# Kernel optimization log

Hardware: AMD Instinct MI355X
Metric: run time of the kernel (lower is better)

## Reference

```python
import jax, jax.numpy as jnp
import numpy as np
from jax import lax

F1, D, F2 = 8, 2, 16
CTX = 64           # context = 1.0 s * 64 Hz
NCH = 64           # EEG channels
POOL1, POOL2 = 2, 5
BN_EPS = 1e-5


def _conv2d(x, w, b, padding, groups=1):
    y = lax.conv_general_dilated(x, w, (1, 1), padding,
                                 dimension_numbers=('NCHW', 'OIHW', 'NCHW'),
                                 feature_group_count=groups)
    return y + b[None, :, None, None]


def _bn(x, g, b, m, v):
    scale = g / jnp.sqrt(v + BN_EPS)
    return (x - m[None, :, None, None]) * scale[None, :, None, None] + b[None, :, None, None]


def _avgpool_w(x, k):
    y = lax.reduce_window(x, jnp.float32(0), lax.add, (1, 1, 1, k), (1, 1, 1, k), 'VALID')
    return y / k


def setup_inputs() -> dict:
    key = jax.random.key(0)
    ks = jax.random.split(key, 24)
    B, C, eegL = 16, NCH, 256
    f32 = jnp.float32
    inp = {
        'eeg': jax.random.normal(ks[0], (B, C, eegL), f32),
        'env': jax.random.normal(ks[1], (B, 2, eegL), f32),
        # conv1: Conv2d(1, F1, (1,3), padding='same')
        'conv1_w': jax.random.normal(ks[2], (F1, 1, 1, 3), f32) * 0.3,
        'conv1_b': jax.random.normal(ks[3], (F1,), f32) * 0.05,
        'bn1_g': jax.random.uniform(ks[4], (F1,), f32, 0.8, 1.2),
        'bn1_b': jax.random.normal(ks[5], (F1,), f32) * 0.05,
        'bn1_m': jax.random.normal(ks[6], (F1,), f32) * 0.1,
        'bn1_v': jax.random.uniform(ks[7], (F1,), f32, 0.5, 1.5),
        # conv2: Conv2d(F1, F1*D, (NCH,1), 'valid', groups=F1)
        'conv2_w': jax.random.normal(ks[8], (F1 * D, 1, NCH, 1), f32) * 0.05,
        'conv2_b': jax.random.normal(ks[9], (F1 * D,), f32) * 0.05,
        'bn2_g': jax.random.uniform(ks[10], (F1 * D,), f32, 0.8, 1.2),
        'bn2_b': jax.random.normal(ks[11], (F1 * D,), f32) * 0.05,
        'bn2_m': jax.random.normal(ks[12], (F1 * D,), f32) * 0.1,
        'bn2_v': jax.random.uniform(ks[13], (F1 * D,), f32, 0.5, 1.5),
        # conv3: depthwise Conv2d(F1*D, F1*D, (1,3), 'same', groups=F1*D)
        'conv3_w': jax.random.normal(ks[14], (F1 * D, 1, 1, 3), f32) * 0.3,
        'conv3_b': jax.random.normal(ks[15], (F1 * D,), f32) * 0.05,
        # conv4: pointwise Conv2d(F1*D, F2, (1,1))
        'conv4_w': jax.random.normal(ks[16], (F2, F1 * D, 1, 1), f32) * 0.2,
        'conv4_b': jax.random.normal(ks[17], (F2,), f32) * 0.05,
        'bn3_g': jax.random.uniform(ks[18], (F2,), f32, 0.8, 1.2),
        'bn3_b': jax.random.normal(ks[19], (F2,), f32) * 0.05,
        'bn3_m': jax.random.normal(ks[20], (F2,), f32) * 0.1,
        'bn3_v': jax.random.uniform(ks[21], (F2,), f32, 0.5, 1.5),
        # linear: F2 * (CTX // (POOL1*POOL2)) -> 1
        'lin_w': jax.random.normal(ks[22], (1, F2 * (CTX // (POOL1 * POOL2))), f32) * 0.1,
        'lin_b': jax.random.normal(ks[23], (1,), f32) * 0.05,
    }
    return inp


def _forward(eeg, conv1_w, conv1_b, bn1_g, bn1_b, bn1_m, bn1_v,
             conv2_w, conv2_b, bn2_g, bn2_b, bn2_m, bn2_v,
             conv3_w, conv3_b, conv4_w, conv4_b,
             bn3_g, bn3_b, bn3_m, bn3_v, lin_w, lin_b):
    B, C, eegL = eeg.shape
    L = eegL - CTX + 1
    # extract all overlapping windows: [B, C, L, CTX] -> [B*L, 1, C, CTX]
    idx = jnp.arange(L)[:, None] + jnp.arange(CTX)[None, :]
    win = eeg[:, :, idx]                      # [B, C, L, CTX]
    x = win.transpose(0, 2, 1, 3).reshape(B * L, 1, C, CTX)
    x = _conv2d(x, conv1_w, conv1_b, ((0, 0), (1, 1)))            # same pad on time
    x = _bn(x, bn1_g, bn1_b, bn1_m, bn1_v)
    x = _conv2d(x, conv2_w, conv2_b, ((0, 0), (0, 0)), groups=F1)  # spatial conv -> H=1
    x = _bn(x, bn2_g, bn2_b, bn2_m, bn2_v)
    x = jax.nn.elu(x)
    x = _avgpool_w(x, POOL1)
    x = _conv2d(x, conv3_w, conv3_b, ((0, 0), (1, 1)), groups=F1 * D)  # depthwise temporal
    x = _conv2d(x, conv4_w, conv4_b, ((0, 0), (0, 0)))                 # pointwise
    x = _bn(x, bn3_g, bn3_b, bn3_m, bn3_v)
    x = jax.nn.elu(x)
    x = _avgpool_w(x, POOL2)
    x = x.reshape(B * L, -1)                  # [B*L, F2*6]
    y = x @ lin_w.T + lin_b                   # [B*L, 1]
    return y.reshape(B, L)


def reference(eeg, env, conv1_w, conv1_b, bn1_g, bn1_b, bn1_m, bn1_v,
              conv2_w, conv2_b, bn2_g, bn2_b, bn2_m, bn2_v,
              conv3_w, conv3_b, conv4_w, conv4_b,
              bn3_g, bn3_b, bn3_m, bn3_v, lin_w, lin_b):
    assert env.shape[1] == 2  # n_streams check (env unused by the math)
    return _forward(eeg, conv1_w, conv1_b, bn1_g, bn1_b, bn1_m, bn1_v,
                    conv2_w, conv2_b, bn2_g, bn2_b, bn2_m, bn2_v,
                    conv3_w, conv3_b, conv4_w, conv4_b,
                    bn3_g, bn3_b, bn3_m, bn3_v, lin_w, lin_b)
```

## Files before the change

### kernel.cpp

```cpp
#include <hip/hip_runtime.h>
#include <math.h>

#define BN_EPS 1e-5f
#define LWIN   193
#define WPB    16
#define NBL    13
#define SLOC   96
#define STR    97

typedef __attribute__((address_space(1))) const unsigned int gl_u32;
typedef __attribute__((address_space(3))) unsigned int lds_u32;

__device__ __forceinline__ float elu(float x) { return x > 0.f ? x : expm1f(x); }

__global__ __launch_bounds__(256) void eegnet_fused(
    const float* __restrict__ eeg,
    const float* __restrict__ c1w, const float* __restrict__ c1b,
    const float* __restrict__ bn1g, const float* __restrict__ bn1b,
    const float* __restrict__ bn1m, const float* __restrict__ bn1v,
    const float* __restrict__ w2,  const float* __restrict__ c2b,
    const float* __restrict__ bn2g, const float* __restrict__ bn2b,
    const float* __restrict__ bn2m, const float* __restrict__ bn2v,
    const float* __restrict__ c3w, const float* __restrict__ c3b,
    const float* __restrict__ c4w, const float* __restrict__ c4b,
    const float* __restrict__ bn3g, const float* __restrict__ bn3b,
    const float* __restrict__ bn3m, const float* __restrict__ bn3v,
    const float* __restrict__ linw, const float* __restrict__ linb,
    float* __restrict__ out)
{
    const int b   = blockIdx.x;
    const int L0  = blockIdx.y * WPB;
    const int g0  = L0 - 3;
    const int tid = threadIdx.x;
    const int lane16 = tid & 15;
    const int grp16  = tid >> 4;

    __shared__ __align__(16) float Eg[64 * SLOC];
    __shared__ float4 w2t4[64 * 4];
    __shared__ float  Ul[16][STR];
    __shared__ float  El[16][STR];
    __shared__ float  P2[16][STR];
    __shared__ float  Ql[16][STR];
    __shared__ float  Ef[16][STR];
    __shared__ float  S5[16][STR];
    __shared__ float  cs[512];
    __shared__ float  q0s[16][17], q1s[16][17];

    const float* ebase = eeg + b * 64 * 256;

    {
        const int wv = tid >> 6, ln = tid & 63;
        #pragma unroll
        for (int j = 0; j < 6; ++j) {
            const int n    = wv * 6 + j;
            const int fidx = n * 256 + ln * 4;
            const int c    = fidx / SLOC;
            const int i    = fidx - c * SLOC;
            const int s    = g0 + i;
            if (s >= 0 && s <= 252) {
                __builtin_amdgcn_global_load_lds((gl_u32*)(ebase + c * 256 + s),
                                                 (lds_u32*)&Eg[n * 256], 16, 0, 0);
            } else {
                const float* row = ebase + c * 256;
                const int e0 = s     < 0 ? 0 : (s     > 255 ? 255 : s);
                const int e1 = s + 1 < 0 ? 0 : (s + 1 > 255 ? 255 : s + 1);
                const int e2 = s + 2 < 0 ? 0 : (s + 2 > 255 ? 255 : s + 2);
                const int e3 = s + 3 < 0 ? 0 : (s + 3 > 255 ? 255 : s + 3);
                *reinterpret_cast<float4*>(&Eg[fidx]) =
                    make_float4(row[e0], row[e1], row[e2], row[e3]);
            }
        }
    }

    {
        const int og = tid >> 6, c = tid & 63, o0 = og * 4;
        w2t4[c * 4 + og] = make_float4(w2[(o0    ) * 64 + c], w2[(o0 + 1) * 64 + c],
                                       w2[(o0 + 2) * 64 + c], w2[(o0 + 3) * 64 + c]);
    }

    if (tid < 64) {
        const int f = tid & 15, q = tid >> 4;
        float s2p = 0.f;
        #pragma unroll
        for (int k = 0; k < 16; ++k) s2p += w2[f * 64 + q * 16 + k];
        s2p += __shfl_xor(s2p, 16);
        s2p += __shfl_xor(s2p, 32);
        if (tid < 16) {
            const int g = f >> 1;
            const float s1 = bn1g[g] / sqrtf(bn1v[g] + BN_EPS);
            const float o1 = bn1b[g] - bn1m[g] * s1;
            const float s2 = bn2g[f] / sqrtf(bn2v[f] + BN_EPS);
            const float o2 = bn2b[f] - bn2m[f] * s2;
            const float ss = s2 * s1;
            cs[      f] = ss * c1w[g * 3 + 0];
            cs[ 16 + f] = ss * c1w[g * 3 + 1];
            cs[ 32 + f] = ss * c1w[g * 3 + 2];
            cs[ 48 + f] = s2 * (fmaf(s1, c1b[g], o1) * s2p + c2b[f]) + o2;
            cs[ 64 + f] = c3w[f * 3 + 0];
            cs[ 80 + f] = c3w[f * 3 + 1];
            cs[ 96 + f] = c3w[f * 3 + 2];
            cs[112 + f] = c3b[f];
        }
    } else if (tid < 128) {
        const int j = tid - 64, f = j & 15, quad = j >> 4;
        const float s3 = bn3g[f] / sqrtf(bn3v[f] + BN_EPS);
        if (quad == 0)
            cs[128 + f] = fmaf(s3, c4b[f], bn3b[f] - bn3m[f] * s3);
        #pragma unroll
        for (int k = 0; k < 4; ++k) {
            const int o = quad * 4 + k;
            cs[144 + o * 16 + f] = s3 * c4w[f * 16 + o];
        }
    } else if (tid < 224) {
        cs[400 + tid - 128] = linw[tid - 128];
    } else if (tid == 224) {
        cs[496] = linb[0];
    }
    __syncthreads();

    {
        const int p  = tid & 63;
        const int og = tid >> 6;
        const bool two = (p < 32);
        float a0 = 0.f, a1 = 0.f, a2 = 0.f, a3 = 0.f;
        float b0 = 0.f, b1 = 0.f, b2 = 0.f, b3 = 0.f;
        #pragma unroll 8
        for (int c = 0; c < 64; ++c) {
            const float4 w = w2t4[c * 4 + og];
            const float  e = Eg[c * SLOC + p];
            a0 = fmaf(w.x, e, a0); a1 = fmaf(w.y, e, a1);
            a2 = fmaf(w.z, e, a2); a3 = fmaf(w.w, e, a3);
            if (two) {
                const float e2 = Eg[c * SLOC + p + 64];
                b0 = fmaf(w.x, e2, b0); b1 = fmaf(w.y, e2, b1);
                b2 = fmaf(w.z, e2, b2); b3 = fmaf(w.w, e2, b3);
            }
        }
        const int o0 = og * 4;
        Ul[o0    ][p] = a0; Ul[o0 + 1][p] = a1;
        Ul[o0 + 2][p] = a2; Ul[o0 + 3][p] = a3;
        if (two) {
            Ul[o0    ][p + 64] = b0; Ul[o0 + 1][p + 64] = b1;
            Ul[o0 + 2][p + 64] = b2; Ul[o0 + 3][p + 64] = b3;
        }
    }
    __syncthreads();

    #pragma unroll
    for (int k = 0; k < 6; ++k) {
        const int i = grp16 + 16 * k, sg = g0 + i, o = lane16;
        const float um = (sg >= 1)   ? Ul[o][i > 0 ? i - 1 : 0] : 0.f;
        const float uc = Ul[o][i];
        const float up = (sg <= 254) ? Ul[o][i < SLOC - 1 ? i + 1 : SLOC - 1] : 0.f;
        El[o][i] = elu(fmaf(cs[o], um, fmaf(cs[16 + o], uc, fmaf(cs[32 + o], up, cs[48 + o]))));
    }
    __syncthreads();

    #pragma unroll
    for (int k = 0; k < 6; ++k) {
        const int i = grp16 + 16 * k, o = lane16;
        const int ip = i < SLOC - 1 ? i + 1 : SLOC - 1;
        P2[o][i] = 0.5f * (El[o][i] + El[o][ip]);
    }
    __syncthreads();

    #pragma unroll
    for (int k = 0; k < 6; ++k) {
        const int i = grp16 + 16 * k, o = lane16;
        const int im = i >= 2 ? i - 2 : 0;
        const int ip = i < SLOC - 2 ? i + 2 : SLOC - 1;
        Ql[o][i] = fmaf(cs[64 + o], P2[o][im],
                   fmaf(cs[80 + o], P2[o][i],
                   fmaf(cs[96 + o], P2[o][ip], cs[112 + o])));
    }
    __syncthreads();

    #pragma unroll
    for (int k = 0; k < 6; ++k) {
        const int i = grp16 + 16 * k, f = lane16;
        float r = cs[128 + f];
        #pragma unroll
        for (int o = 0; o < 16; ++o)
            r = fmaf(cs[144 + o * 16 + f], Ql[o][i], r);
        Ef[f][i] = elu(r);
    }
    __syncthreads();

    #pragma unroll
    for (int k = 0; k < 6; ++k) {
        const int i = grp16 + 16 * k, f = lane16;
        const int i2 = i + 2 < SLOC ? i + 2 : SLOC - 1;
        const int i4 = i + 4 < SLOC ? i + 4 : SLOC - 1;
        const int i6 = i + 6 < SLOC ? i + 6 : SLOC - 1;
        const int i8 = i + 8 < SLOC ? i + 8 : SLOC - 1;
        S5[f][i] = Ef[f][i] + Ef[f][i2] + Ef[f][i4] + Ef[f][i6] + Ef[f][i8];
    }
    __syncthreads();

    {
        const int w = grp16, o = lane16, l = L0 + w;
        if (l < LWIN) {
            const int li = w + 3;
            const float z0 = fmaf(cs[16 + o], Ul[o][li], fmaf(cs[32 + o], Ul[o][li + 1], cs[48 + o]));
            const float P0 = 0.5f * (elu(z0) + El[o][li + 1]);
            const float pa = P2[o][li + 2], pb = P2[o][li + 4];
            q0s[w][o] = fmaf(cs[80 + o], P0, fmaf(cs[96 + o], pa, cs[112 + o]));
            q1s[w][o] = fmaf(cs[64 + o], P0, fmaf(cs[80 + o], pa, fmaf(cs[96 + o], pb, cs[112 + o])));
        }
    }
    __syncthreads();

    {
        const int w = grp16, f = lane16, l = L0 + w;
        float part = 0.f;
        if (l < LWIN) {
            const int li = w + 3;
            float r0 = cs[128 + f], r1 = r0;
            #pragma unroll
            for (int o = 0; o < 16; ++o) {
                const float wt = cs[144 + o * 16 + f];
                r0 = fmaf(wt, q0s[w][o], r0);
                r1 = fmaf(wt, q1s[w][o], r1);
            }
            part = cs[400 + f * 6] * (elu(r0) + elu(r1) - Ef[f][li] - Ef[f][li + 2]);
            #pragma unroll
            for (int g = 0; g < 6; ++g)
                part = fmaf(cs[400 + f * 6 + g], S5[f][li + 10 * g], part);
        }
        part += __shfl_xor(part, 1);
        part += __shfl_xor(part, 2);
        part += __shfl_xor(part, 4);
        part += __shfl_xor(part, 8);
        if (f == 0 && l < LWIN) out[b * LWIN + l] = fmaf(0.2f, part, cs[496]);
    }
}

extern "C" void kernel_launch(void* const* d_in, const int* in_sizes, int n_in,
                              void* d_out, int out_size, void* d_ws, size_t ws_size,
                              hipStream_t stream) {
    const float* eeg  = (const float*)d_in[0];
    const float* c1w  = (const float*)d_in[2];
    const float* c1b  = (const float*)d_in[3];
    const float* bn1g = (const float*)d_in[4];
    const float* bn1b = (const float*)d_in[5];
    const float* bn1m = (const float*)d_in[6];
    const float* bn1v = (const float*)d_in[7];
    const float* w2   = (const float*)d_in[8];
    const float* c2b  = (const float*)d_in[9];
    const float* bn2g = (const float*)d_in[10];
    const float* bn2b = (const float*)d_in[11];
    const float* bn2m = (const float*)d_in[12];
    const float* bn2v = (const float*)d_in[13];
    const float* c3w  = (const float*)d_in[14];
    const float* c3b  = (const float*)d_in[15];
    const float* c4w  = (const float*)d_in[16];
    const float* c4b  = (const float*)d_in[17];
    const float* bn3g = (const float*)d_in[18];
    const float* bn3b = (const float*)d_in[19];
    const float* bn3m = (const float*)d_in[20];
    const float* bn3v = (const float*)d_in[21];
    const float* linw = (const float*)d_in[22];
    const float* linb = (const float*)d_in[23];

    eegnet_fused<<<dim3(16, NBL), 256, 0, stream>>>(
        eeg, c1w, c1b, bn1g, bn1b, bn1m, bn1v, w2, c2b,
        bn2g, bn2b, bn2m, bn2v, c3w, c3b, c4w, c4b,
        bn3g, bn3b, bn3m, bn3v, linw, linb, (float*)d_out);
}
```

Before: 15.58 us.

## Split fused kernel into per-position stage and per-window stage via workspace

```diff
diff --git a/kernel.cpp b/kernel.cpp
--- a/kernel.cpp
+++ b/kernel.cpp
@@ -5,15 +5,17 @@
 #define LWIN   193
 #define WPB    16
 #define NBL    13
-#define SLOC   96
-#define STR    97
+#define CPOS   32
+#define NCHK   8
+#define LLOC   48
+#define ASTR   49
 
 typedef __attribute__((address_space(1))) const unsigned int gl_u32;
 typedef __attribute__((address_space(3))) unsigned int lds_u32;
 
 __device__ __forceinline__ float elu(float x) { return x > 0.f ? x : expm1f(x); }
 
-__global__ __launch_bounds__(256) void eegnet_fused(
+__global__ __launch_bounds__(256) void eegnet_stage1(
     const float* __restrict__ eeg,
     const float* __restrict__ c1w, const float* __restrict__ c1b,
     const float* __restrict__ bn1g, const float* __restrict__ bn1b,
@@ -26,37 +28,34 @@
     const float* __restrict__ bn3g, const float* __restrict__ bn3b,
     const float* __restrict__ bn3m, const float* __restrict__ bn3v,
     const float* __restrict__ linw, const float* __restrict__ linb,
-    float* __restrict__ out)
+    float* __restrict__ cstg, float* __restrict__ P0g, float* __restrict__ P2g,
+    float* __restrict__ Efg, float* __restrict__ S5g)
 {
-    const int b   = blockIdx.x;
-    const int L0  = blockIdx.y * WPB;
-    const int g0  = L0 - 3;
-    const int tid = threadIdx.x;
+    const int b     = blockIdx.x;
+    const int cb    = blockIdx.y;
+    const int sbase = cb * CPOS;
+    const int l0    = sbase - 3;
+    const int tid   = threadIdx.x;
     const int lane16 = tid & 15;
     const int grp16  = tid >> 4;
 
-    __shared__ __align__(16) float Eg[64 * SLOC];
+    __shared__ __align__(16) float Eg[64 * LLOC];
     __shared__ float4 w2t4[64 * 4];
-    __shared__ float  Ul[16][STR];
-    __shared__ float  El[16][STR];
-    __shared__ float  P2[16][STR];
-    __shared__ float  Ql[16][STR];
-    __shared__ float  Ef[16][STR];
-    __shared__ float  S5[16][STR];
+    __shared__ float  Ul[16][ASTR], El[16][ASTR], EZ[16][ASTR], P2[16][ASTR];
+    __shared__ float  Ql[16][ASTR], Ef[16][ASTR], S5[16][ASTR], P0[16][ASTR];
     __shared__ float  cs[512];
-    __shared__ float  q0s[16][17], q1s[16][17];
 
     const float* ebase = eeg + b * 64 * 256;
 
     {
         const int wv = tid >> 6, ln = tid & 63;
         #pragma unroll
-        for (int j = 0; j < 6; ++j) {
-            const int n    = wv * 6 + j;
+        for (int j = 0; j < 3; ++j) {
+            const int n    = wv * 3 + j;
             const int fidx = n * 256 + ln * 4;
-            const int c    = fidx / SLOC;
-            const int i    = fidx - c * SLOC;
-            const int s    = g0 + i;
+            const int c    = fidx / LLOC;
+            const int i    = fidx - c * LLOC;
+            const int s    = l0 + i;
             if (s >= 0 && s <= 252) {
                 __builtin_amdgcn_global_load_lds((gl_u32*)(ebase + c * 256 + s),
                                                  (lds_u32*)&Eg[n * 256], 16, 0, 0);
@@ -115,60 +114,58 @@
         cs[400 + tid - 128] = linw[tid - 128];
     } else if (tid == 224) {
         cs[496] = linb[0];
-    }
-    __syncthreads();
-
-    {
-        const int p  = tid & 63;
-        const int og = tid >> 6;
-        const bool two = (p < 32);
-        float a0 = 0.f, a1 = 0.f, a2 = 0.f, a3 = 0.f;
-        float b0 = 0.f, b1 = 0.f, b2 = 0.f, b3 = 0.f;
-        #pragma unroll 8
-        for (int c = 0; c < 64; ++c) {
-            const float4 w = w2t4[c * 4 + og];
-            const float  e = Eg[c * SLOC + p];
-            a0 = fmaf(w.x, e, a0); a1 = fmaf(w.y, e, a1);
-            a2 = fmaf(w.z, e, a2); a3 = fmaf(w.w, e, a3);
-            if (two) {
-                const float e2 = Eg[c * SLOC + p + 64];
-                b0 = fmaf(w.x, e2, b0); b1 = fmaf(w.y, e2, b1);
-                b2 = fmaf(w.z, e2, b2); b3 = fmaf(w.w, e2, b3);
+    } else if (tid < 240) {
+        cs[tid + 272] = 0.f;
+    }
+    __syncthreads();
+
+    if (b == 0 && cb == 0)
+        for (int idx = tid; idx < 512; idx += 256) cstg[idx] = cs[idx];
+
+    {
+        const int p = tid & 63, og = tid >> 6;
+        if (p < LLOC) {
+            float a0 = 0.f, a1 = 0.f, a2 = 0.f, a3 = 0.f;
+            #pragma unroll 8
+            for (int c = 0; c < 64; ++c) {
+                const float4 w = w2t4[c * 4 + og];
+                const float  e = Eg[c * LLOC + p];
+                a0 = fmaf(w.x, e, a0); a1 = fmaf(w.y, e, a1);
+                a2 = fmaf(w.z, e, a2); a3 = fmaf(w.w, e, a3);
             }
-        }
-        const int o0 = og * 4;
-        Ul[o0    ][p] = a0; Ul[o0 + 1][p] = a1;
-        Ul[o0 + 2][p] = a2; Ul[o0 + 3][p] = a3;
-        if (two) {
-            Ul[o0    ][p + 64] = b0; Ul[o0 + 1][p + 64] = b1;
-            Ul[o0 + 2][p + 64] = b2; Ul[o0 + 3][p + 64] = b3;
-        }
-    }
-    __syncthreads();
-
-    #pragma unroll
-    for (int k = 0; k < 6; ++k) {
-        const int i = grp16 + 16 * k, sg = g0 + i, o = lane16;
+            const int o0 = og * 4;
+            Ul[o0    ][p] = a0; Ul[o0 + 1][p] = a1;
+            Ul[o0 + 2][p] = a2; Ul[o0 + 3][p] = a3;
+        }
+    }
+    __syncthreads();
+
+    #pragma unroll
+    for (int k = 0; k < 3; ++k) {
+        const int i = grp16 + 16 * k, sg = l0 + i, o = lane16;
         const float um = (sg >= 1)   ? Ul[o][i > 0 ? i - 1 : 0] : 0.f;
         const float uc = Ul[o][i];
-        const float up = (sg <= 254) ? Ul[o][i < SLOC - 1 ? i + 1 : SLOC - 1] : 0.f;
-        El[o][i] = elu(fmaf(cs[o], um, fmaf(cs[16 + o], uc, fmaf(cs[32 + o], up, cs[48 + o]))));
-    }
-    __syncthreads();
-
-    #pragma unroll
-    for (int k = 0; k < 6; ++k) {
+        const float up = (sg <= 254) ? Ul[o][i < LLOC - 1 ? i + 1 : LLOC - 1] : 0.f;
+        const float t  = fmaf(cs[16 + o], uc, fmaf(cs[32 + o], up, cs[48 + o]));
+        El[o][i] = elu(fmaf(cs[o], um, t));
+        EZ[o][i] = elu(t);
+    }
+    __syncthreads();
+
+    #pragma unroll
+    for (int k = 0; k < 3; ++k) {
         const int i = grp16 + 16 * k, o = lane16;
-        const int ip = i < SLOC - 1 ? i + 1 : SLOC - 1;
+        const int ip = i < LLOC - 1 ? i + 1 : LLOC - 1;
         P2[o][i] = 0.5f * (El[o][i] + El[o][ip]);
-    }
-    __syncthreads();
-
-    #pragma unroll
-    for (int k = 0; k < 6; ++k) {
+        P0[o][i] = 0.5f * (EZ[o][i] + El[o][ip]);
+    }
+    __syncthreads();
+
+    #pragma unroll
+    for (int k = 0; k < 3; ++k) {
         const int i = grp16 + 16 * k, o = lane16;
         const int im = i >= 2 ? i - 2 : 0;
-        const int ip = i < SLOC - 2 ? i + 2 : SLOC - 1;
+        const int ip = i < LLOC - 2 ? i + 2 : LLOC - 1;
         Ql[o][i] = fmaf(cs[64 + o], P2[o][im],
                    fmaf(cs[80 + o], P2[o][i],
                    fmaf(cs[96 + o], P2[o][ip], cs[112 + o])));
@@ -176,7 +173,7 @@
     __syncthreads();
 
     #pragma unroll
-    for (int k = 0; k < 6; ++k) {
+    for (int k = 0; k < 3; ++k) {
         const int i = grp16 + 16 * k, f = lane16;
         float r = cs[128 + f];
         #pragma unroll
@@ -187,25 +184,85 @@
     __syncthreads();
 
     #pragma unroll
-    for (int k = 0; k < 6; ++k) {
+    for (int k = 0; k < 3; ++k) {
         const int i = grp16 + 16 * k, f = lane16;
-        const int i2 = i + 2 < SLOC ? i + 2 : SLOC - 1;
-        const int i4 = i + 4 < SLOC ? i + 4 : SLOC - 1;
-        const int i6 = i + 6 < SLOC ? i + 6 : SLOC - 1;
-        const int i8 = i + 8 < SLOC ? i + 8 : SLOC - 1;
+        const int i2 = i + 2 < LLOC ? i + 2 : LLOC - 1;
+        const int i4 = i + 4 < LLOC ? i + 4 : LLOC - 1;
+        const int i6 = i + 6 < LLOC ? i + 6 : LLOC - 1;
+        const int i8 = i + 8 < LLOC ? i + 8 : LLOC - 1;
         S5[f][i] = Ef[f][i] + Ef[f][i2] + Ef[f][i4] + Ef[f][i6] + Ef[f][i8];
+    }
+    __syncthreads();
+
+    {
+        const int o = tid >> 4, j = tid & 15, i0 = 3 + 2 * j;
+        const int gidx = (b * 16 + o) * 256 + sbase + 2 * j;
+        float2 v;
+        v.x = P0[o][i0]; v.y = P0[o][i0 + 1]; *reinterpret_cast<float2*>(&P0g[gidx]) = v;
+        v.x = P2[o][i0]; v.y = P2[o][i0 + 1]; *reinterpret_cast<float2*>(&P2g[gidx]) = v;
+        v.x = Ef[o][i0]; v.y = Ef[o][i0 + 1]; *reinterpret_cast<float2*>(&Efg[gidx]) = v;
+        v.x = S5[o][i0]; v.y = S5[o][i0 + 1]; *reinterpret_cast<float2*>(&S5g[gidx]) = v;
+    }
+}
+
+__global__ __launch_bounds__(256) void eegnet_stage2(
+    const float* __restrict__ cstg, const float* __restrict__ P0g,
+    const float* __restrict__ P2g, const float* __restrict__ Efg,
+    const float* __restrict__ S5g, float* __restrict__ out)
+{
+    const int b   = blockIdx.x;
+    const int L0  = blockIdx.y * WPB;
+    const int tid = threadIdx.x;
+    const int lane16 = tid & 15;
+    const int grp16  = tid >> 4;
+
+    __shared__ __align__(16) float csB[512];
+    __shared__ __align__(16) float P0l[16 * 20];
+    __shared__ __align__(16) float P2l[16 * 20];
+    __shared__ __align__(16) float Efl[16 * 20];
+    __shared__ __align__(16) float S5l[16 * 68];
+    __shared__ float q0s[16][17], q1s[16][17];
+
+    {
+        const int wv = tid >> 6, ln = tid & 63;
+        const int rowbase = b * 16;
+        for (int t = wv; t < 13; t += 4) {
+            if (t < 2) {
+                __builtin_amdgcn_global_load_lds((gl_u32*)(cstg + t * 256 + ln * 4),
+                                                 (lds_u32*)&csB[t * 256], 16, 0, 0);
+            } else if (t < 8) {
+                const int a = (t - 2) >> 1, half = (t - 2) & 1;
+                const float* g = a == 0 ? P0g : (a == 1 ? P2g : Efg);
+                float* l = a == 0 ? P0l : (a == 1 ? P2l : Efl);
+                const int m = half * 64 + ln;
+                if (m < 80) {
+                    const int row = m / 5, cc = m - row * 5;
+                    __builtin_amdgcn_global_load_lds(
+                        (gl_u32*)(g + (rowbase + row) * 256 + L0 + cc * 4),
+                        (lds_u32*)&l[half * 256], 16, 0, 0);
+                }
+            } else {
+                const int j = t - 8;
+                const int m = j * 64 + ln;
+                if (m < 272) {
+                    const int row = m / 17, cc = m - row * 17;
+                    __builtin_amdgcn_global_load_lds(
+                        (gl_u32*)(S5g + (rowbase + row) * 256 + L0 + cc * 4),
+                        (lds_u32*)&S5l[j * 256], 16, 0, 0);
+                }
+            }
+        }
     }
     __syncthreads();
 
     {
         const int w = grp16, o = lane16, l = L0 + w;
         if (l < LWIN) {
-            const int li = w + 3;
-            const float z0 = fmaf(cs[16 + o], Ul[o][li], fmaf(cs[32 + o], Ul[o][li + 1], cs[48 + o]));
-            const float P0 = 0.5f * (elu(z0) + El[o][li + 1]);
-            const float pa = P2[o][li + 2], pb = P2[o][li + 4];
-            q0s[w][o] = fmaf(cs[80 + o], P0, fmaf(cs[96 + o], pa, cs[112 + o]));
-            q1s[w][o] = fmaf(cs[64 + o], P0, fmaf(cs[80 + o], pa, fmaf(cs[96 + o], pb, cs[112 + o])));
+            const float P0v = P0l[o * 20 + w];
+            const float pa  = P2l[o * 20 + w + 2], pb = P2l[o * 20 + w + 4];
+            q0s[w][o] = fmaf(csB[80 + o], P0v, fmaf(csB[96 + o], pa, csB[112 + o]));
+            q1s[w][o] = fmaf(csB[64 + o], P0v,
+                        fmaf(csB[80 + o], pa, fmaf(csB[96 + o], pb, csB[112 + o])));
         }
     }
     __syncthreads();
@@ -214,24 +271,24 @@
         const int w = grp16, f = lane16, l = L0 + w;
         float part = 0.f;
         if (l < LWIN) {
-            const int li = w + 3;
-            float r0 = cs[128 + f], r1 = r0;
+            float r0 = csB[128 + f], r1 = r0;
             #pragma unroll
             for (int o = 0; o < 16; ++o) {
-                const float wt = cs[144 + o * 16 + f];
+                const float wt = csB[144 + o * 16 + f];
                 r0 = fmaf(wt, q0s[w][o], r0);
                 r1 = fmaf(wt, q1s[w][o], r1);
             }
-            part = cs[400 + f * 6] * (elu(r0) + elu(r1) - Ef[f][li] - Ef[f][li + 2]);
+            part = csB[400 + f * 6] *
+                   (elu(r0) + elu(r1) - Efl[f * 20 + w] - Efl[f * 20 + w + 2]);
             #pragma unroll
             for (int g = 0; g < 6; ++g)
-                part = fmaf(cs[400 + f * 6 + g], S5[f][li + 10 * g], part);
+                part = fmaf(csB[400 + f * 6 + g], S5l[f * 68 + w + 10 * g], part);
         }
         part += __shfl_xor(part, 1);
         part += __shfl_xor(part, 2);
         part += __shfl_xor(part, 4);
         part += __shfl_xor(part, 8);
-        if (f == 0 && l < LWIN) out[b * LWIN + l] = fmaf(0.2f, part, cs[496]);
+        if (f == 0 && l < LWIN) out[b * LWIN + l] = fmaf(0.2f, part, csB[496]);
     }
 }
 
@@ -262,8 +319,18 @@
     const float* linw = (const float*)d_in[22];
     const float* linb = (const float*)d_in[23];
 
-    eegnet_fused<<<dim3(16, NBL), 256, 0, stream>>>(
+    float* cstg = (float*)d_ws;
+    float* P0g  = cstg + 512;
+    float* P2g  = P0g + 65536;
+    float* Efg  = P2g + 65536;
+    float* S5g  = Efg + 65536;
+
+    eegnet_stage1<<<dim3(16, NCHK), 256, 0, stream>>>(
         eeg, c1w, c1b, bn1g, bn1b, bn1m, bn1v, w2, c2b,
         bn2g, bn2b, bn2m, bn2v, c3w, c3b, c4w, c4b,
-        bn3g, bn3b, bn3m, bn3v, linw, linb, (float*)d_out);
+        bn3g, bn3b, bn3m, bn3v, linw, linb,
+        cstg, P0g, P2g, Efg, S5g);
+
+    eegnet_stage2<<<dim3(16, NBL), 256, 0, stream>>>(
+        cstg, P0g, P2g, Efg, S5g, (float*)d_out);
 }
```

After: 18.27 us. +17.2%, slower.

## Double block to 512 threads and merge pooling/depthwise and tail stages

Applied to the files above, without the earlier changes.

```diff
diff --git a/kernel.cpp b/kernel.cpp
--- a/kernel.cpp
+++ b/kernel.cpp
@@ -13,7 +13,7 @@
 
 __device__ __forceinline__ float elu(float x) { return x > 0.f ? x : expm1f(x); }
 
-__global__ __launch_bounds__(256) void eegnet_fused(
+__global__ __launch_bounds__(512) void eegnet_fused(
     const float* __restrict__ eeg,
     const float* __restrict__ c1w, const float* __restrict__ c1b,
     const float* __restrict__ bn1g, const float* __restrict__ bn1b,
@@ -33,16 +33,11 @@
     const int g0  = L0 - 3;
     const int tid = threadIdx.x;
     const int lane16 = tid & 15;
-    const int grp16  = tid >> 4;
+    const int grp32  = tid >> 4;
 
     __shared__ __align__(16) float Eg[64 * SLOC];
-    __shared__ float4 w2t4[64 * 4];
-    __shared__ float  Ul[16][STR];
-    __shared__ float  El[16][STR];
-    __shared__ float  P2[16][STR];
-    __shared__ float  Ql[16][STR];
-    __shared__ float  Ef[16][STR];
-    __shared__ float  S5[16][STR];
+    __shared__ float2 w2t2[64 * 8];
+    __shared__ float  Ul[16][STR], El[16][STR], Ql[16][STR], Ef[16][STR];
     __shared__ float  cs[512];
     __shared__ float  q0s[16][17], q1s[16][17];
 
@@ -51,8 +46,8 @@
     {
         const int wv = tid >> 6, ln = tid & 63;
         #pragma unroll
-        for (int j = 0; j < 6; ++j) {
-            const int n    = wv * 6 + j;
+        for (int j = 0; j < 3; ++j) {
+            const int n    = wv * 3 + j;
             const int fidx = n * 256 + ln * 4;
             const int c    = fidx / SLOC;
             const int i    = fidx - c * SLOC;
@@ -73,9 +68,9 @@
     }
 
     {
-        const int og = tid >> 6, c = tid & 63, o0 = og * 4;
-        w2t4[c * 4 + og] = make_float4(w2[(o0    ) * 64 + c], w2[(o0 + 1) * 64 + c],
-                                       w2[(o0 + 2) * 64 + c], w2[(o0 + 3) * 64 + c]);
+        const int o8 = tid >> 6, c = tid & 63;
+        w2t2[c * 8 + o8] = make_float2(w2[(2 * o8    ) * 64 + c],
+                                       w2[(2 * o8 + 1) * 64 + c]);
     }
 
     if (tid < 64) {
@@ -119,36 +114,28 @@
     __syncthreads();
 
     {
-        const int p  = tid & 63;
-        const int og = tid >> 6;
+        const int p = tid & 63, o8 = tid >> 6;
         const bool two = (p < 32);
-        float a0 = 0.f, a1 = 0.f, a2 = 0.f, a3 = 0.f;
-        float b0 = 0.f, b1 = 0.f, b2 = 0.f, b3 = 0.f;
+        float a0 = 0.f, a1 = 0.f, b0 = 0.f, b1 = 0.f;
         #pragma unroll 8
         for (int c = 0; c < 64; ++c) {
-            const float4 w = w2t4[c * 4 + og];
+            const float2 w = w2t2[c * 8 + o8];
             const float  e = Eg[c * SLOC + p];
             a0 = fmaf(w.x, e, a0); a1 = fmaf(w.y, e, a1);
-            a2 = fmaf(w.z, e, a2); a3 = fmaf(w.w, e, a3);
             if (two) {
                 const float e2 = Eg[c * SLOC + p + 64];
                 b0 = fmaf(w.x, e2, b0); b1 = fmaf(w.y, e2, b1);
-                b2 = fmaf(w.z, e2, b2); b3 = fmaf(w.w, e2, b3);
-            }
-        }
-        const int o0 = og * 4;
-        Ul[o0    ][p] = a0; Ul[o0 + 1][p] = a1;
-        Ul[o0 + 2][p] = a2; Ul[o0 + 3][p] = a3;
-        if (two) {
-            Ul[o0    ][p + 64] = b0; Ul[o0 + 1][p + 64] = b1;
-            Ul[o0 + 2][p + 64] = b2; Ul[o0 + 3][p + 64] = b3;
-        }
+            }
+        }
+        const int o0 = 2 * o8;
+        Ul[o0][p] = a0; Ul[o0 + 1][p] = a1;
+        if (two) { Ul[o0][p + 64] = b0; Ul[o0 + 1][p + 64] = b1; }
     }
     __syncthreads();
 
     #pragma unroll
-    for (int k = 0; k < 6; ++k) {
-        const int i = grp16 + 16 * k, sg = g0 + i, o = lane16;
+    for (int k = 0; k < 3; ++k) {
+        const int i = grp32 + 32 * k, sg = g0 + i, o = lane16;
         const float um = (sg >= 1)   ? Ul[o][i > 0 ? i - 1 : 0] : 0.f;
         const float uc = Ul[o][i];
         const float up = (sg <= 254) ? Ul[o][i < SLOC - 1 ? i + 1 : SLOC - 1] : 0.f;
@@ -156,28 +143,41 @@
     }
     __syncthreads();
 
+    {
+        const int o = lane16;
+        #pragma unroll
+        for (int k = 0; k < 3; ++k) {
+            const int i  = grp32 + 32 * k;
+            const int im = i >= 2 ? i - 2 : 0;
+            const int ip = i < SLOC - 2 ? i + 2 : SLOC - 1;
+            const float pm = 0.5f * (El[o][im] + El[o][im < SLOC - 1 ? im + 1 : SLOC - 1]);
+            const float pc = 0.5f * (El[o][i ] + El[o][i  < SLOC - 1 ? i  + 1 : SLOC - 1]);
+            const float pp = 0.5f * (El[o][ip] + El[o][ip < SLOC - 1 ? ip + 1 : SLOC - 1]);
+            Ql[o][i] = fmaf(cs[64 + o], pm,
+                       fmaf(cs[80 + o], pc,
+                       fmaf(cs[96 + o], pp, cs[112 + o])));
+        }
+        const int w = grp32 & 15, half = grp32 >> 4, l = L0 + w;
+        if (l < LWIN) {
+            const int li = w + 3;
+            const float z0 = fmaf(cs[16 + o], Ul[o][li],
+                             fmaf(cs[32 + o], Ul[o][li + 1], cs[48 + o]));
+            const float P0 = 0.5f * (elu(z0) + El[o][li + 1]);
+            const float pa = 0.5f * (El[o][li + 2] + El[o][li + 3]);
+            if (half == 0) {
+                q0s[w][o] = fmaf(cs[80 + o], P0, fmaf(cs[96 + o], pa, cs[112 + o]));
+            } else {
+                const float pb = 0.5f * (El[o][li + 4] + El[o][li + 5]);
+                q1s[w][o] = fmaf(cs[64 + o], P0,
+                            fmaf(cs[80 + o], pa, fmaf(cs[96 + o], pb, cs[112 + o])));
+            }
+        }
+    }
+    __syncthreads();
+
     #pragma unroll
-    for (int k = 0; k < 6; ++k) {
-        const int i = grp16 + 16 * k, o = lane16;
-        const int ip = i < SLOC - 1 ? i + 1 : SLOC - 1;
-        P2[o][i] = 0.5f * (El[o][i] + El[o][ip]);
-    }
-    __syncthreads();
-
-    #pragma unroll
-    for (int k = 0; k < 6; ++k) {
-        const int i = grp16 + 16 * k, o = lane16;
-        const int im = i >= 2 ? i - 2 : 0;
-        const int ip = i < SLOC - 2 ? i + 2 : SLOC - 1;
-        Ql[o][i] = fmaf(cs[64 + o], P2[o][im],
-                   fmaf(cs[80 + o], P2[o][i],
-                   fmaf(cs[96 + o], P2[o][ip], cs[112 + o])));
-    }
-    __syncthreads();
-
-    #pragma unroll
-    for (int k = 0; k < 6; ++k) {
-        const int i = grp16 + 16 * k, f = lane16;
+    for (int k = 0; k < 3; ++k) {
+        const int i = grp32 + 32 * k, f = lane16;
         float r = cs[128 + f];
         #pragma unroll
         for (int o = 0; o < 16; ++o)
@@ -186,52 +186,34 @@
     }
     __syncthreads();
 
-    #pragma unroll
-    for (int k = 0; k < 6; ++k) {
-        const int i = grp16 + 16 * k, f = lane16;
-        const int i2 = i + 2 < SLOC ? i + 2 : SLOC - 1;
-        const int i4 = i + 4 < SLOC ? i + 4 : SLOC - 1;
-        const int i6 = i + 6 < SLOC ? i + 6 : SLOC - 1;
-        const int i8 = i + 8 < SLOC ? i + 8 : SLOC - 1;
-        S5[f][i] = Ef[f][i] + Ef[f][i2] + Ef[f][i4] + Ef[f][i6] + Ef[f][i8];
-    }
-    __syncthreads();
-
-    {
-        const int w = grp16, o = lane16, l = L0 + w;
-        if (l < LWIN) {
-            const int li = w + 3;
-            const float z0 = fmaf(cs[16 + o], Ul[o][li], fmaf(cs[32 + o], Ul[o][li + 1], cs[48 + o]));
-            const float P0 = 0.5f * (elu(z0) + El[o][li + 1]);
-            const float pa = P2[o][li + 2], pb = P2[o][li + 4];
-            q0s[w][o] = fmaf(cs[80 + o], P0, fmaf(cs[96 + o], pa, cs[112 + o]));
-            q1s[w][o] = fmaf(cs[64 + o], P0, fmaf(cs[80 + o], pa, fmaf(cs[96 + o], pb, cs[112 + o])));
-        }
-    }
-    __syncthreads();
-
-    {
-        const int w = grp16, f = lane16, l = L0 + w;
+    {
+        const int w = tid >> 5, lane32 = tid & 31;
+        const int f = lane32 & 15, h = lane32 >> 4;
+        const int l = L0 + w;
         float part = 0.f;
         if (l < LWIN) {
             const int li = w + 3;
-            float r0 = cs[128 + f], r1 = r0;
+            float r = cs[128 + f];
+            const float* q = h ? &q1s[w][0] : &q0s[w][0];
             #pragma unroll
-            for (int o = 0; o < 16; ++o) {
-                const float wt = cs[144 + o * 16 + f];
-                r0 = fmaf(wt, q0s[w][o], r0);
-                r1 = fmaf(wt, q1s[w][o], r1);
-            }
-            part = cs[400 + f * 6] * (elu(r0) + elu(r1) - Ef[f][li] - Ef[f][li + 2]);
+            for (int o = 0; o < 16; ++o)
+                r = fmaf(cs[144 + o * 16 + f], q[o], r);
+            part = cs[400 + f * 6] * (elu(r) - Ef[f][li + 2 * h]);
             #pragma unroll
-            for (int g = 0; g < 6; ++g)
-                part = fmaf(cs[400 + f * 6 + g], S5[f][li + 10 * g], part);
+            for (int gg = 0; gg < 3; ++gg) {
+                const int g = h * 3 + gg;
+                const int p0 = li + 10 * g;
+                const float s5 = Ef[f][p0] + Ef[f][p0 + 2] + Ef[f][p0 + 4]
+                               + Ef[f][p0 + 6] + Ef[f][p0 + 8];
+                part = fmaf(cs[400 + f * 6 + g], s5, part);
+            }
         }
         part += __shfl_xor(part, 1);
         part += __shfl_xor(part, 2);
         part += __shfl_xor(part, 4);
         part += __shfl_xor(part, 8);
-        if (f == 0 && l < LWIN) out[b * LWIN + l] = fmaf(0.2f, part, cs[496]);
+        part += __shfl_xor(part, 16);
+        if (lane32 == 0 && l < LWIN) out[b * LWIN + l] = fmaf(0.2f, part, cs[496]);
     }
 }
 
@@ -262,7 +244,7 @@
     const float* linw = (const float*)d_in[22];
     const float* linb = (const float*)d_in[23];
 
-    eegnet_fused<<<dim3(16, NBL), 256, 0, stream>>>(
+    eegnet_fused<<<dim3(16, NBL), 512, 0, stream>>>(
         eeg, c1w, c1b, bn1g, bn1b, bn1m, bn1v, w2, c2b,
         bn2g, bn2b, bn2m, bn2v, c3w, c3b, c4w, c4b,
         bn3g, bn3b, bn3m, bn3v, linw, linb, (float*)d_out);
```

New measurement: 19.85 us. 1.27x slower.

## Fuse pipeline stages to cut block barriers and intermediate LDS buffers

Applied to the files above, without the earlier changes.

```diff
diff --git a/kernel.cpp b/kernel.cpp
--- a/kernel.cpp
+++ b/kernel.cpp
@@ -37,22 +37,16 @@
 
     __shared__ __align__(16) float Eg[64 * SLOC];
     __shared__ float4 w2t4[64 * 4];
-    __shared__ float  Ul[16][STR];
-    __shared__ float  El[16][STR];
-    __shared__ float  P2[16][STR];
-    __shared__ float  Ql[16][STR];
-    __shared__ float  Ef[16][STR];
-    __shared__ float  S5[16][STR];
+    __shared__ float  Ul[16][STR], El[16][STR], Ql[16][STR], Ef[16][STR];
     __shared__ float  cs[512];
-    __shared__ float  q0s[16][17], q1s[16][17];
+    __shared__ __align__(16) float q0s[16][20], q1s[16][20];
 
     const float* ebase = eeg + b * 64 * 256;
 
     {
-        const int wv = tid >> 6, ln = tid & 63;
-        #pragma unroll
-        for (int j = 0; j < 6; ++j) {
-            const int n    = wv * 6 + j;
+        const int ln = tid & 63;
+        #pragma unroll
+        for (int n = 0; n < 24; ++n) {
             const int fidx = n * 256 + ln * 4;
             const int c    = fidx / SLOC;
             const int i    = fidx - c * SLOC;
@@ -76,6 +70,36 @@
         const int og = tid >> 6, c = tid & 63, o0 = og * 4;
         w2t4[c * 4 + og] = make_float4(w2[(o0    ) * 64 + c], w2[(o0 + 1) * 64 + c],
                                        w2[(o0 + 2) * 64 + c], w2[(o0 + 3) * 64 + c]);
+    }
+
+    asm volatile("s_waitcnt vmcnt(0) lgkmcnt(0)" ::: "memory");
+    __builtin_amdgcn_sched_barrier(0);
+
+    {
+        const int p  = tid & 63;
+        const int og = tid >> 6;
+        const bool two = (p < 32);
+        float a0 = 0.f, a1 = 0.f, a2 = 0.f, a3 = 0.f;
+        float b0 = 0.f, b1 = 0.f, b2 = 0.f, b3 = 0.f;
+        #pragma unroll 8
+        for (int c = 0; c < 64; ++c) {
+            const float4 w = w2t4[c * 4 + og];
+            const float  e = Eg[c * SLOC + p];
+            a0 = fmaf(w.x, e, a0); a1 = fmaf(w.y, e, a1);
+            a2 = fmaf(w.z, e, a2); a3 = fmaf(w.w, e, a3);
+            if (two) {
+                const float e2 = Eg[c * SLOC + p + 64];
+                b0 = fmaf(w.x, e2, b0); b1 = fmaf(w.y, e2, b1);
+                b2 = fmaf(w.z, e2, b2); b3 = fmaf(w.w, e2, b3);
+            }
+        }
+        const int o0 = og * 4;
+        Ul[o0    ][p] = a0; Ul[o0 + 1][p] = a1;
+        Ul[o0 + 2][p] = a2; Ul[o0 + 3][p] = a3;
+        if (two) {
+            Ul[o0    ][p + 64] = b0; Ul[o0 + 1][p + 64] = b1;
+            Ul[o0 + 2][p + 64] = b2; Ul[o0 + 3][p + 64] = b3;
+        }
     }
 
     if (tid < 64) {
@@ -118,34 +142,6 @@
     }
     __syncthreads();
 
-    {
-        const int p  = tid & 63;
-        const int og = tid >> 6;
-        const bool two = (p < 32);
-        float a0 = 0.f, a1 = 0.f, a2 = 0.f, a3 = 0.f;
-        float b0 = 0.f, b1 = 0.f, b2 = 0.f, b3 = 0.f;
-        #pragma unroll 8
-        for (int c = 0; c < 64; ++c) {
-            const float4 w = w2t4[c * 4 + og];
-            const float  e = Eg[c * SLOC + p];
-            a0 = fmaf(w.x, e, a0); a1 = fmaf(w.y, e, a1);
-            a2 = fmaf(w.z, e, a2); a3 = fmaf(w.w, e, a3);
-            if (two) {
-                const float e2 = Eg[c * SLOC + p + 64];
-                b0 = fmaf(w.x, e2, b0); b1 = fmaf(w.y, e2, b1);
-                b2 = fmaf(w.z, e2, b2); b3 = fmaf(w.w, e2, b3);
-            }
-        }
-        const int o0 = og * 4;
-        Ul[o0    ][p] = a0; Ul[o0 + 1][p] = a1;
-        Ul[o0 + 2][p] = a2; Ul[o0 + 3][p] = a3;
-        if (two) {
-            Ul[o0    ][p + 64] = b0; Ul[o0 + 1][p + 64] = b1;
-            Ul[o0 + 2][p + 64] = b2; Ul[o0 + 3][p + 64] = b3;
-        }
-    }
-    __syncthreads();
-
     #pragma unroll
     for (int k = 0; k < 6; ++k) {
         const int i = grp16 + 16 * k, sg = g0 + i, o = lane16;
@@ -156,22 +152,32 @@
     }
     __syncthreads();
 
-    #pragma unroll
-    for (int k = 0; k < 6; ++k) {
-        const int i = grp16 + 16 * k, o = lane16;
-        const int ip = i < SLOC - 1 ? i + 1 : SLOC - 1;
-        P2[o][i] = 0.5f * (El[o][i] + El[o][ip]);
-    }
-    __syncthreads();
-
-    #pragma unroll
-    for (int k = 0; k < 6; ++k) {
-        const int i = grp16 + 16 * k, o = lane16;
-        const int im = i >= 2 ? i - 2 : 0;
-        const int ip = i < SLOC - 2 ? i + 2 : SLOC - 1;
-        Ql[o][i] = fmaf(cs[64 + o], P2[o][im],
-                   fmaf(cs[80 + o], P2[o][i],
-                   fmaf(cs[96 + o], P2[o][ip], cs[112 + o])));
+    {
+        const int o = lane16;
+        #pragma unroll
+        for (int k = 0; k < 6; ++k) {
+            const int i  = grp16 + 16 * k;
+            const int im = i >= 2 ? i - 2 : 0;
+            const int ip = i < SLOC - 2 ? i + 2 : SLOC - 1;
+            const float pm = 0.5f * (El[o][im] + El[o][im < SLOC - 1 ? im + 1 : SLOC - 1]);
+            const float pc = 0.5f * (El[o][i ] + El[o][i  < SLOC - 1 ? i  + 1 : SLOC - 1]);
+            const float pp = 0.5f * (El[o][ip] + El[o][ip < SLOC - 1 ? ip + 1 : SLOC - 1]);
+            Ql[o][i] = fmaf(cs[64 + o], pm,
+                       fmaf(cs[80 + o], pc,
+                       fmaf(cs[96 + o], pp, cs[112 + o])));
+        }
+        const int w = grp16, l = L0 + w;
+        if (l < LWIN) {
+            const int li = w + 3;
+            const float z0 = fmaf(cs[16 + o], Ul[o][li],
+                             fmaf(cs[32 + o], Ul[o][li + 1], cs[48 + o]));
+            const float P0 = 0.5f * (elu(z0) + El[o][li + 1]);
+            const float pa = 0.5f * (El[o][li + 2] + El[o][li + 3]);
+            const float pb = 0.5f * (El[o][li + 4] + El[o][li + 5]);
+            q0s[w][o] = fmaf(cs[80 + o], P0, fmaf(cs[96 + o], pa, cs[112 + o]));
+            q1s[w][o] = fmaf(cs[64 + o], P0,
+                        fmaf(cs[80 + o], pa, fmaf(cs[96 + o], pb, cs[112 + o])));
+        }
     }
     __syncthreads();
 
@@ -183,30 +189,6 @@
         for (int o = 0; o < 16; ++o)
             r = fmaf(cs[144 + o * 16 + f], Ql[o][i], r);
         Ef[f][i] = elu(r);
-    }
-    __syncthreads();
-
-    #pragma unroll
-    for (int k = 0; k < 6; ++k) {
-        const int i = grp16 + 16 * k, f = lane16;
-        const int i2 = i + 2 < SLOC ? i + 2 : SLOC - 1;
-        const int i4 = i + 4 < SLOC ? i + 4 : SLOC - 1;
-        const int i6 = i + 6 < SLOC ? i + 6 : SLOC - 1;
-        const int i8 = i + 8 < SLOC ? i + 8 : SLOC - 1;
-        S5[f][i] = Ef[f][i] + Ef[f][i2] + Ef[f][i4] + Ef[f][i6] + Ef[f][i8];
-    }
-    __syncthreads();
-
-    {
-        const int w = grp16, o = lane16, l = L0 + w;
-        if (l < LWIN) {
-            const int li = w + 3;
-            const float z0 = fmaf(cs[16 + o], Ul[o][li], fmaf(cs[32 + o], Ul[o][li + 1], cs[48 + o]));
-            const float P0 = 0.5f * (elu(z0) + El[o][li + 1]);
-            const float pa = P2[o][li + 2], pb = P2[o][li + 4];
-            q0s[w][o] = fmaf(cs[80 + o], P0, fmaf(cs[96 + o], pa, cs[112 + o]));
-            q1s[w][o] = fmaf(cs[64 + o], P0, fmaf(cs[80 + o], pa, fmaf(cs[96 + o], pb, cs[112 + o])));
-        }
     }
     __syncthreads();
 
@@ -216,16 +198,28 @@
         if (l < LWIN) {
             const int li = w + 3;
             float r0 = cs[128 + f], r1 = r0;
+            const float4* q04 = reinterpret_cast<const float4*>(&q0s[w][0]);
+            const float4* q14 = reinterpret_cast<const float4*>(&q1s[w][0]);
             #pragma unroll
-            for (int o = 0; o < 16; ++o) {
-                const float wt = cs[144 + o * 16 + f];
-                r0 = fmaf(wt, q0s[w][o], r0);
-                r1 = fmaf(wt, q1s[w][o], r1);
+            for (int ov = 0; ov < 4; ++ov) {
+                const float4 a = q04[ov], c = q14[ov];
+                r0 = fmaf(cs[144 + (4*ov    ) * 16 + f], a.x, r0);
+                r0 = fmaf(cs[144 + (4*ov + 1) * 16 + f], a.y, r0);
+                r0 = fmaf(cs[144 + (4*ov + 2) * 16 + f], a.z, r0);
+                r0 = fmaf(cs[144 + (4*ov + 3) * 16 + f], a.w, r0);
+                r1 = fmaf(cs[144 + (4*ov    ) * 16 + f], c.x, r1);
+                r1 = fmaf(cs[144 + (4*ov + 1) * 16 + f], c.y, r1);
+                r1 = fmaf(cs[144 + (4*ov + 2) * 16 + f], c.z, r1);
+                r1 = fmaf(cs[144 + (4*ov + 3) * 16 + f], c.w, r1);
             }
             part = cs[400 + f * 6] * (elu(r0) + elu(r1) - Ef[f][li] - Ef[f][li + 2]);
             #pragma unroll
-            for (int g = 0; g < 6; ++g)
-                part = fmaf(cs[400 + f * 6 + g], S5[f][li + 10 * g], part);
+            for (int g = 0; g < 6; ++g) {
+                const int p0 = li + 10 * g;
+                const float s5 = Ef[f][p0] + Ef[f][p0 + 2] + Ef[f][p0 + 4]
+                               + Ef[f][p0 + 6] + Ef[f][p0 + 8];
+                part = fmaf(cs[400 + f * 6 + g], s5, part);
+            }
         }
         part += __shfl_xor(part, 1);
         part += __shfl_xor(part, 2);
```

Result: slower. 19.14 us (+22.9%).
